# Kernel tuning notes

Measured on AMD Instinct MI355X. Metric: run time of the kernel, lower is better.

The kernel has to match this reference:

```python
import jax, jax.numpy as jnp
import numpy as np

B, C, Hs, Ws = 8, 512, 32, 32
NUM_HEADS, D_K = 8, 64
SCALE = D_K ** -0.5


def setup_inputs() -> dict:
    key = jax.random.key(0)
    ks = jax.random.split(key, 8)
    inner = NUM_HEADS * D_K  # 512
    s = 0.02
    return {
        "x": jax.random.normal(ks[0], (B, C, Hs, Ws), dtype=jnp.float32),
        "y": jax.random.normal(ks[1], (B, C, Hs, Ws), dtype=jnp.float32),
        "Wq": jax.random.normal(ks[2], (inner, C), dtype=jnp.float32) * s,
        "bq": jnp.zeros((inner,), dtype=jnp.float32),
        "Wkv": jax.random.normal(ks[3], (2 * inner, C), dtype=jnp.float32) * s,
        "bkv": jnp.zeros((2 * inner,), dtype=jnp.float32),
        "Wp": jax.random.normal(ks[4], (C, inner), dtype=jnp.float32) * s,
        "bp": jnp.zeros((C,), dtype=jnp.float32),
    }


def reference(x, y, Wq, bq, Wkv, bkv, Wp, bp):
    # Faithful to CrossAttentionBlock.forward: y is only shape-checked, unused.
    x_shape = x.shape
    b, c = x.shape[0], x.shape[1]
    # channel_transfer: [B, C, H, W] -> [B, H, W, C] -> [B, N, C]
    xt = jnp.transpose(x, (0, 2, 3, 1)).reshape(b, -1, c)
    n = xt.shape[1]
    # q: [B, N, H*dk] -> [B, H, N, dk]
    q = (xt @ Wq.T + bq).reshape(b, n, NUM_HEADS, D_K).transpose(0, 2, 1, 3)
    # kv: [B, N, 2*H*dk] -> [2, B, H, N, dk]
    kv = (xt @ Wkv.T + bkv).reshape(b, n, 2, NUM_HEADS, D_K).transpose(2, 0, 3, 1, 4)
    k, v = kv[0], kv[1]
    atten = jnp.einsum("bhik,bhjk->bhij", q, k) * SCALE
    atten = jax.nn.softmax(atten, axis=-1)
    res = jnp.einsum("bhij,bhjd->bhid", atten, v)  # [B, H, N, dk]
    res = res.transpose(0, 2, 1, 3).reshape(b, n, NUM_HEADS * D_K)
    res = res @ Wp.T + bp  # [B, N, C]
    # original does a raw reshape of [B, N, C] back into x_shape [B, C, H, W]
    return res.reshape(x_shape)
```

## Files before the change

### kernel.cpp

```cpp
#include <hip/hip_runtime.h>
#include <math.h>

#define BB 8
#define CC 512
#define NH 8
#define DK 64
#define NN 1024
#define MROWS (BB * NN)
#define INNER 512
#define SCALE 0.125f

typedef __attribute__((ext_vector_type(8))) short bf16x8;
typedef __attribute__((ext_vector_type(4))) float floatx4;

__device__ inline short f2bf(float f) {
    union { float f; unsigned u; } un;
    un.f = f;
    unsigned r = un.u + 0x7fffu + ((un.u >> 16) & 1u);
    return (short)(r >> 16);
}

__device__ inline short f2bf_rhu(float f) {
    union { float f; unsigned u; } un;
    un.f = f;
    return (short)((un.u + 0x8000u) >> 16);
}

#define GLD_LDS(gptr, lptr)                                                  \
    __builtin_amdgcn_global_load_lds(                                        \
        (const __attribute__((address_space(1))) void*)(gptr),               \
        (__attribute__((address_space(3))) void*)(lptr), 16, 0, 0)

__global__ __launch_bounds__(256) void xt_transpose_kernel(
    const float* __restrict__ x, short* __restrict__ xt) {
    __shared__ float tile[32][33];
    const int b = blockIdx.z;
    const int c0 = blockIdx.y * 32;
    const int n0 = blockIdx.x * 32;
    const float* xb = x + (size_t)b * CC * NN;
    short* xtb = xt + (size_t)b * NN * CC;
    const int tx = threadIdx.x;
    for (int i = threadIdx.y; i < 32; i += 8) {
        tile[i][tx] = xb[(size_t)(c0 + i) * NN + n0 + tx];
    }
    __syncthreads();
    for (int i = threadIdx.y; i < 32; i += 8) {
        xtb[(size_t)(n0 + i) * CC + c0 + tx] = f2bf(tile[tx][i]);
    }
}

__global__ __launch_bounds__(256) void cvt_all_kernel(
    const float* __restrict__ Wq, const float* __restrict__ Wkv,
    const float* __restrict__ Wp, const float* __restrict__ bq,
    const float* __restrict__ bkv, short* __restrict__ wqkvb,
    short* __restrict__ wpb, float* __restrict__ bqkv) {
    const int i = (blockIdx.x * 256 + threadIdx.x) * 4;
    if (i < 786432) {
        float4 v = (i < 262144) ? *(const float4*)&Wq[i]
                                : *(const float4*)&Wkv[i - 262144];
        wqkvb[i + 0] = f2bf(v.x);
        wqkvb[i + 1] = f2bf(v.y);
        wqkvb[i + 2] = f2bf(v.z);
        wqkvb[i + 3] = f2bf(v.w);
    } else if (i < 1048576) {
        const int j = i - 786432;
        float4 v = *(const float4*)&Wp[j];
        wpb[j + 0] = f2bf(v.x);
        wpb[j + 1] = f2bf(v.y);
        wpb[j + 2] = f2bf(v.z);
        wpb[j + 3] = f2bf(v.w);
    } else {
        const int j = i - 1048576;
        if (j < 1536) {
            float4 v = (j < 512) ? *(const float4*)&bq[j]
                                 : *(const float4*)&bkv[j - 512];
            *(float4*)&bqkv[j] = v;
        }
    }
}

template <int MODE>
__global__ __launch_bounds__(256) void gemm_mfma_kernel(
    const short* __restrict__ A, const short* __restrict__ W,
    const float* __restrict__ bias, float* __restrict__ outf,
    short* __restrict__ outq, short* __restrict__ outk,
    short* __restrict__ outv) {
    constexpr int K = 512;
    __shared__ short As[128 * 32];
    __shared__ short Bs[128 * 32];

    const int t = threadIdx.x;
    const int wave = t >> 6;
    const int lane = t & 63;
    const int col = lane & 15;
    const int quad = lane >> 4;
    const int wr = wave >> 1;
    const int wc = wave & 1;

    const int bm0 = blockIdx.y * 128;
    const int bn0 = blockIdx.x * 128;

    floatx4 acc[4][4];
#pragma unroll
    for (int i = 0; i < 4; i++)
#pragma unroll
        for (int j = 0; j < 4; j++) acc[i][j] = (floatx4){0.f, 0.f, 0.f, 0.f};

    const int rA = wave * 32 + (lane >> 2);
    const int kpE = (lane & 3) * 8;
    const short* Ag = A + (size_t)(bm0 + rA) * K + kpE;
    const short* Wg = W + (size_t)(bn0 + rA) * K + kpE;
    short* AsW = As + wave * 1024;
    short* BsW = Bs + wave * 1024;

    for (int k0 = 0; k0 < K; k0 += 32) {
        __syncthreads();
        GLD_LDS(Ag + k0, AsW);
        GLD_LDS(Ag + 16 * K + k0, AsW + 512);
        GLD_LDS(Wg + k0, BsW);
        GLD_LDS(Wg + 16 * K + k0, BsW + 512);
        __syncthreads();

        bf16x8 aF[4], bF[4];
#pragma unroll
        for (int rt = 0; rt < 4; rt++)
            aF[rt] = *(const bf16x8*)&As[(wr * 64 + rt * 16 + col) * 32 + quad * 8];
#pragma unroll
        for (int ct = 0; ct < 4; ct++)
            bF[ct] = *(const bf16x8*)&Bs[(wc * 64 + ct * 16 + col) * 32 + quad * 8];
#pragma unroll
        for (int rt = 0; rt < 4; rt++)
#pragma unroll
            for (int ct = 0; ct < 4; ct++)
                acc[rt][ct] = __builtin_amdgcn_mfma_f32_16x16x32_bf16(
                    aF[rt], bF[ct], acc[rt][ct], 0, 0, 0);
    }

#pragma unroll
    for (int rt = 0; rt < 4; rt++) {
#pragma unroll
        for (int ct = 0; ct < 4; ct++) {
            const int jn = bn0 + wc * 64 + ct * 16 + col;
            const float bsv = bias[jn];
#pragma unroll
            for (int r = 0; r < 4; r++) {
                const int m = bm0 + wr * 64 + rt * 16 + quad * 4 + r;
                const float val = acc[rt][ct][r] + bsv;
                if (MODE == 0) {
                    outf[(size_t)m * 512 + jn] = val;
                } else {
                    const int b = m >> 10;
                    const int n = m & 1023;
                    const int reg = jn >> 9;
                    const int h = (jn >> 6) & 7;
                    const int d = jn & 63;
                    if (reg == 0)
                        outq[(((size_t)(b * NH + h)) * NN + n) * DK + d] =
                            f2bf(val * SCALE);
                    else if (reg == 1)
                        outk[(((size_t)(b * NH + h)) * NN + n) * DK + d] = f2bf(val);
                    else
                        outv[(((size_t)(b * NH + h)) * DK + d) * NN + n] = f2bf(val);
                }
            }
        }
    }
}

__global__ __launch_bounds__(512) void attn_mfma_kernel(
    const short* __restrict__ q, const short* __restrict__ k,
    const short* __restrict__ vt, short* __restrict__ out) {
    const int bh = blockIdx.y;
    const int b = bh >> 3;
    const int h = bh & 7;
    const int n0 = blockIdx.x * 128;
    const int tid = threadIdx.x;
    const int wave = tid >> 6;
    const int lane = tid & 63;
    const int col = lane & 15;
    const int quad = lane >> 4;

    __shared__ short Ks[64 * 64];
    __shared__ short Vs[64 * 64];
    __shared__ short Ps[8][16][72];

    bf16x8 qa0, qa1;
    {
        const size_t qoff = ((size_t)bh * NN + n0 + wave * 16 + col) * DK;
        qa0 = *(const bf16x8*)&q[qoff + quad * 8];
        qa1 = *(const bf16x8*)&q[qoff + 32 + quad * 8];
    }

    floatx4 o[4];
#pragma unroll
    for (int i = 0; i < 4; i++) o[i] = (floatx4){0.f, 0.f, 0.f, 0.f};
    float l_run[4] = {0.f, 0.f, 0.f, 0.f};

    const short* kg = k + (size_t)bh * NN * DK;
    const short* vg = vt + (size_t)bh * DK * NN;

    const int srow = lane >> 3;
    const int sunit = (lane & 7) ^ srow;
    const int sbase = (wave & 3) * 16;

    const int xs = col & 7;
    const int pK0 = (quad ^ xs) * 8;
    const int pK1 = ((quad + 4) ^ xs) * 8;

    for (int j0 = 0; j0 < NN; j0 += 64) {
        __syncthreads();
        if (wave < 4) {
            GLD_LDS(kg + (size_t)(j0 + sbase + srow) * DK + sunit * 8,
                    &Ks[sbase * 64]);
            GLD_LDS(kg + (size_t)(j0 + sbase + 8 + srow) * DK + sunit * 8,
                    &Ks[(sbase + 8) * 64]);
        } else {
            GLD_LDS(vg + (size_t)(sbase + srow) * NN + j0 + sunit * 8,
                    &Vs[sbase * 64]);
            GLD_LDS(vg + (size_t)(sbase + 8 + srow) * NN + j0 + sunit * 8,
                    &Vs[(sbase + 8) * 64]);
        }
        __syncthreads();

        float p[4][4];
#pragma unroll
        for (int ct = 0; ct < 4; ct++) {
            bf16x8 kb0 = *(const bf16x8*)&Ks[(ct * 16 + col) * 64 + pK0];
            bf16x8 kb1 = *(const bf16x8*)&Ks[(ct * 16 + col) * 64 + pK1];
            floatx4 acc = (floatx4){0.f, 0.f, 0.f, 0.f};
            acc = __builtin_amdgcn_mfma_f32_16x16x32_bf16(qa0, kb0, acc, 0, 0, 0);
            acc = __builtin_amdgcn_mfma_f32_16x16x32_bf16(qa1, kb1, acc, 0, 0, 0);
#pragma unroll
            for (int r = 0; r < 4; r++) p[ct][r] = __expf(acc[r]);
        }

#pragma unroll
        for (int r = 0; r < 4; r++)
            l_run[r] += (p[0][r] + p[1][r]) + (p[2][r] + p[3][r]);

#pragma unroll
        for (int ct = 0; ct < 4; ct++)
#pragma unroll
            for (int r = 0; r < 4; r++)
                Ps[wave][quad * 4 + r][ct * 16 + col] = f2bf_rhu(p[ct][r]);

        bf16x8 pa0 = *(const bf16x8*)&Ps[wave][col][quad * 8];
        bf16x8 pa1 = *(const bf16x8*)&Ps[wave][col][32 + quad * 8];

#pragma unroll
        for (int dt = 0; dt < 4; dt++) {
            bf16x8 vb0 = *(const bf16x8*)&Vs[(dt * 16 + col) * 64 + pK0];
            bf16x8 vb1 = *(const bf16x8*)&Vs[(dt * 16 + col) * 64 + pK1];
            o[dt] = __builtin_amdgcn_mfma_f32_16x16x32_bf16(pa0, vb0, o[dt], 0, 0, 0);
            o[dt] = __builtin_amdgcn_mfma_f32_16x16x32_bf16(pa1, vb1, o[dt], 0, 0, 0);
        }
    }

#pragma unroll
    for (int r = 0; r < 4; r++) {
        float lv = l_run[r];
#pragma unroll
        for (int d = 1; d < 16; d <<= 1) lv += __shfl_xor(lv, d, 64);
        const float inv = 1.f / lv;
        const int m = n0 + wave * 16 + quad * 4 + r;
        short* orow = out + ((size_t)(b * NN + m)) * 512 + h * 64;
#pragma unroll
        for (int dt = 0; dt < 4; dt++) orow[dt * 16 + col] = f2bf(o[dt][r] * inv);
    }
}

extern "C" void kernel_launch(void* const* d_in, const int* in_sizes, int n_in,
                              void* d_out, int out_size, void* d_ws,
                              size_t ws_size, hipStream_t stream) {
    const float* x = (const float*)d_in[0];
    const float* Wq = (const float*)d_in[2];
    const float* bq = (const float*)d_in[3];
    const float* Wkv = (const float*)d_in[4];
    const float* bkv = (const float*)d_in[5];
    const float* Wp = (const float*)d_in[6];
    const float* bp = (const float*)d_in[7];
    float* out = (float*)d_out;

    short* ws = (short*)d_ws;
    short* xtb = ws;
    short* qb = xtb + (size_t)MROWS * CC;
    short* kb = qb + (size_t)MROWS * INNER;
    short* vb = kb + (size_t)MROWS * INNER;
    short* wqkvb = vb + (size_t)MROWS * INNER;
    short* wpb = wqkvb + (size_t)3 * INNER * CC;
    float* bqkv = (float*)(wpb + (size_t)CC * INNER);
    short* att = xtb;

    {
        dim3 grid(NN / 32, CC / 32, BB);
        dim3 block(32, 8);
        xt_transpose_kernel<<<grid, block, 0, stream>>>(x, xtb);
    }
    cvt_all_kernel<<<1026, 256, 0, stream>>>(Wq, Wkv, Wp, bq, bkv, wqkvb, wpb,
                                             bqkv);
    {
        dim3 grid((3 * INNER) / 128, MROWS / 128);
        gemm_mfma_kernel<1><<<grid, 256, 0, stream>>>(xtb, wqkvb, bqkv, nullptr,
                                                      qb, kb, vb);
    }
    {
        dim3 grid(NN / 128, BB * NH);
        attn_mfma_kernel<<<grid, 512, 0, stream>>>(qb, kb, vb, att);
    }
    {
        dim3 grid(CC / 128, MROWS / 128);
        gemm_mfma_kernel<0><<<grid, 256, 0, stream>>>(att, wpb, bp, out,
                                                      nullptr, nullptr, nullptr);
    }
}
```

Baseline: 171.1 us.

## Merge prep kernels, double-buffer attention K/V tiles, narrow output GEMM tile

Three separate changes. The transpose and weight-conversion kernels are merged into one launch to save a kernel launch. The attention loop double-buffers the K/V shared-memory tiles so the next tile's global-to-LDS load overlaps compute, which also removes one barrier per iteration. The output projection GEMM now uses a 64-wide N tile, doubling its grid from 256 to 512 blocks to fill more CUs, at the cost of less reuse of A per block.

```diff
diff --git a/kernel.cpp b/kernel.cpp
--- a/kernel.cpp
+++ b/kernel.cpp
@@ -31,105 +31,115 @@
         (const __attribute__((address_space(1))) void*)(gptr),               \
         (__attribute__((address_space(3))) void*)(lptr), 16, 0, 0)
 
-__global__ __launch_bounds__(256) void xt_transpose_kernel(
-    const float* __restrict__ x, short* __restrict__ xt) {
+__global__ __launch_bounds__(256) void prep_kernel(
+    const float* __restrict__ x, const float* __restrict__ Wq,
+    const float* __restrict__ Wkv, const float* __restrict__ Wp,
+    const float* __restrict__ bq, const float* __restrict__ bkv,
+    short* __restrict__ xtb, short* __restrict__ wqkvb,
+    short* __restrict__ wpb, float* __restrict__ bqkv) {
     __shared__ float tile[32][33];
-    const int b = blockIdx.z;
-    const int c0 = blockIdx.y * 32;
-    const int n0 = blockIdx.x * 32;
-    const float* xb = x + (size_t)b * CC * NN;
-    short* xtb = xt + (size_t)b * NN * CC;
-    const int tx = threadIdx.x;
-    for (int i = threadIdx.y; i < 32; i += 8) {
-        tile[i][tx] = xb[(size_t)(c0 + i) * NN + n0 + tx];
-    }
-    __syncthreads();
-    for (int i = threadIdx.y; i < 32; i += 8) {
-        xtb[(size_t)(n0 + i) * CC + c0 + tx] = f2bf(tile[tx][i]);
-    }
-}
-
-__global__ __launch_bounds__(256) void cvt_all_kernel(
-    const float* __restrict__ Wq, const float* __restrict__ Wkv,
-    const float* __restrict__ Wp, const float* __restrict__ bq,
-    const float* __restrict__ bkv, short* __restrict__ wqkvb,
-    short* __restrict__ wpb, float* __restrict__ bqkv) {
-    const int i = (blockIdx.x * 256 + threadIdx.x) * 4;
-    if (i < 786432) {
-        float4 v = (i < 262144) ? *(const float4*)&Wq[i]
-                                : *(const float4*)&Wkv[i - 262144];
-        wqkvb[i + 0] = f2bf(v.x);
-        wqkvb[i + 1] = f2bf(v.y);
-        wqkvb[i + 2] = f2bf(v.z);
-        wqkvb[i + 3] = f2bf(v.w);
-    } else if (i < 1048576) {
-        const int j = i - 786432;
-        float4 v = *(const float4*)&Wp[j];
-        wpb[j + 0] = f2bf(v.x);
-        wpb[j + 1] = f2bf(v.y);
-        wpb[j + 2] = f2bf(v.z);
-        wpb[j + 3] = f2bf(v.w);
+    const int bid = blockIdx.x;
+    if (bid < 4096) {
+        const int n0 = (bid & 31) * 32;
+        const int c0 = ((bid >> 5) & 15) * 32;
+        const int b = bid >> 9;
+        const int tx = threadIdx.x & 31;
+        const int ty = threadIdx.x >> 5;
+        const float* xb = x + (size_t)b * CC * NN;
+        short* xo = xtb + (size_t)b * NN * CC;
+        for (int i = ty; i < 32; i += 8)
+            tile[i][tx] = xb[(size_t)(c0 + i) * NN + n0 + tx];
+        __syncthreads();
+        for (int i = ty; i < 32; i += 8)
+            xo[(size_t)(n0 + i) * CC + c0 + tx] = f2bf(tile[tx][i]);
     } else {
-        const int j = i - 1048576;
-        if (j < 1536) {
-            float4 v = (j < 512) ? *(const float4*)&bq[j]
-                                 : *(const float4*)&bkv[j - 512];
-            *(float4*)&bqkv[j] = v;
-        }
-    }
-}
-
-template <int MODE>
+        const int i = (bid - 4096) * 1024 + threadIdx.x * 4;
+        if (i < 786432) {
+            float4 v = (i < 262144) ? *(const float4*)&Wq[i]
+                                    : *(const float4*)&Wkv[i - 262144];
+            wqkvb[i + 0] = f2bf(v.x);
+            wqkvb[i + 1] = f2bf(v.y);
+            wqkvb[i + 2] = f2bf(v.z);
+            wqkvb[i + 3] = f2bf(v.w);
+        } else if (i < 1048576) {
+            const int j = i - 786432;
+            float4 v = *(const float4*)&Wp[j];
+            wpb[j + 0] = f2bf(v.x);
+            wpb[j + 1] = f2bf(v.y);
+            wpb[j + 2] = f2bf(v.z);
+            wpb[j + 3] = f2bf(v.w);
+        } else {
+            const int j = i - 1048576;
+            if (j < 1536) {
+                float4 v = (j < 512) ? *(const float4*)&bq[j]
+                                     : *(const float4*)&bkv[j - 512];
+                *(float4*)&bqkv[j] = v;
+            }
+        }
+    }
+}
+
+template <int MODE, int BN>
 __global__ __launch_bounds__(256) void gemm_mfma_kernel(
     const short* __restrict__ A, const short* __restrict__ W,
     const float* __restrict__ bias, float* __restrict__ outf,
     short* __restrict__ outq, short* __restrict__ outk,
     short* __restrict__ outv) {
     constexpr int K = 512;
+    constexpr int WCOLS = BN / 64;
+    constexpr int WROWS = 4 / WCOLS;
+    constexpr int WRSPAN = 128 / WROWS;
+    constexpr int RT = WRSPAN / 16;
     __shared__ short As[128 * 32];
-    __shared__ short Bs[128 * 32];
+    __shared__ short Bs[BN * 32];
 
     const int t = threadIdx.x;
     const int wave = t >> 6;
     const int lane = t & 63;
     const int col = lane & 15;
     const int quad = lane >> 4;
-    const int wr = wave >> 1;
-    const int wc = wave & 1;
+    const int wr = wave / WCOLS;
+    const int wc = wave % WCOLS;
 
     const int bm0 = blockIdx.y * 128;
-    const int bn0 = blockIdx.x * 128;
-
-    floatx4 acc[4][4];
-#pragma unroll
-    for (int i = 0; i < 4; i++)
+    const int bn0 = blockIdx.x * BN;
+
+    floatx4 acc[RT][4];
+#pragma unroll
+    for (int i = 0; i < RT; i++)
 #pragma unroll
         for (int j = 0; j < 4; j++) acc[i][j] = (floatx4){0.f, 0.f, 0.f, 0.f};
 
+    const int kpE = (lane & 3) * 8;
     const int rA = wave * 32 + (lane >> 2);
-    const int kpE = (lane & 3) * 8;
     const short* Ag = A + (size_t)(bm0 + rA) * K + kpE;
-    const short* Wg = W + (size_t)(bn0 + rA) * K + kpE;
     short* AsW = As + wave * 1024;
-    short* BsW = Bs + wave * 1024;
+    const int rB = wave * (BN / 4) + (lane >> 2);
+    const short* Wg = W + (size_t)(bn0 + rB) * K + kpE;
+    short* BsW = Bs + wave * (BN / 4) * 32;
 
     for (int k0 = 0; k0 < K; k0 += 32) {
         __syncthreads();
         GLD_LDS(Ag + k0, AsW);
         GLD_LDS(Ag + 16 * K + k0, AsW + 512);
-        GLD_LDS(Wg + k0, BsW);
-        GLD_LDS(Wg + 16 * K + k0, BsW + 512);
+        if constexpr (BN == 128) {
+            GLD_LDS(Wg + k0, BsW);
+            GLD_LDS(Wg + 16 * K + k0, BsW + 512);
+        } else {
+            GLD_LDS(Wg + k0, BsW);
+        }
         __syncthreads();
 
-        bf16x8 aF[4], bF[4];
-#pragma unroll
-        for (int rt = 0; rt < 4; rt++)
-            aF[rt] = *(const bf16x8*)&As[(wr * 64 + rt * 16 + col) * 32 + quad * 8];
+        bf16x8 aF[RT], bF[4];
+#pragma unroll
+        for (int rt = 0; rt < RT; rt++)
+            aF[rt] =
+                *(const bf16x8*)&As[(wr * WRSPAN + rt * 16 + col) * 32 + quad * 8];
 #pragma unroll
         for (int ct = 0; ct < 4; ct++)
             bF[ct] = *(const bf16x8*)&Bs[(wc * 64 + ct * 16 + col) * 32 + quad * 8];
 #pragma unroll
-        for (int rt = 0; rt < 4; rt++)
+        for (int rt = 0; rt < RT; rt++)
 #pragma unroll
             for (int ct = 0; ct < 4; ct++)
                 acc[rt][ct] = __builtin_amdgcn_mfma_f32_16x16x32_bf16(
@@ -137,14 +147,14 @@
     }
 
 #pragma unroll
-    for (int rt = 0; rt < 4; rt++) {
+    for (int rt = 0; rt < RT; rt++) {
 #pragma unroll
         for (int ct = 0; ct < 4; ct++) {
             const int jn = bn0 + wc * 64 + ct * 16 + col;
             const float bsv = bias[jn];
 #pragma unroll
             for (int r = 0; r < 4; r++) {
-                const int m = bm0 + wr * 64 + rt * 16 + quad * 4 + r;
+                const int m = bm0 + wr * WRSPAN + rt * 16 + quad * 4 + r;
                 const float val = acc[rt][ct][r] + bsv;
                 if (MODE == 0) {
                     outf[(size_t)m * 512 + jn] = val;
@@ -180,8 +190,8 @@
     const int col = lane & 15;
     const int quad = lane >> 4;
 
-    __shared__ short Ks[64 * 64];
-    __shared__ short Vs[64 * 64];
+    __shared__ short Ks[2][64 * 64];
+    __shared__ short Vs[2][64 * 64];
     __shared__ short Ps[8][16][72];
 
     bf16x8 qa0, qa1;
@@ -207,26 +217,36 @@
     const int pK0 = (quad ^ xs) * 8;
     const int pK1 = ((quad + 4) ^ xs) * 8;
 
-    for (int j0 = 0; j0 < NN; j0 += 64) {
+#define STAGE(J0, BUF)                                                         \
+    do {                                                                       \
+        if (wave < 4) {                                                        \
+            GLD_LDS(kg + (size_t)((J0) + sbase + srow) * DK + sunit * 8,       \
+                    &Ks[BUF][sbase * 64]);                                     \
+            GLD_LDS(kg + (size_t)((J0) + sbase + 8 + srow) * DK + sunit * 8,   \
+                    &Ks[BUF][(sbase + 8) * 64]);                               \
+        } else {                                                               \
+            GLD_LDS(vg + (size_t)(sbase + srow) * NN + (J0) + sunit * 8,       \
+                    &Vs[BUF][sbase * 64]);                                     \
+            GLD_LDS(vg + (size_t)(sbase + 8 + srow) * NN + (J0) + sunit * 8,   \
+                    &Vs[BUF][(sbase + 8) * 64]);                               \
+        }                                                                      \
+    } while (0)
+
+    STAGE(0, 0);
+
+    for (int c = 0; c < 16; c++) {
+        const int buf = c & 1;
         __syncthreads();
-        if (wave < 4) {
-            GLD_LDS(kg + (size_t)(j0 + sbase + srow) * DK + sunit * 8,
-                    &Ks[sbase * 64]);
-            GLD_LDS(kg + (size_t)(j0 + sbase + 8 + srow) * DK + sunit * 8,
-                    &Ks[(sbase + 8) * 64]);
-        } else {
-            GLD_LDS(vg + (size_t)(sbase + srow) * NN + j0 + sunit * 8,
-                    &Vs[sbase * 64]);
-            GLD_LDS(vg + (size_t)(sbase + 8 + srow) * NN + j0 + sunit * 8,
-                    &Vs[(sbase + 8) * 64]);
-        }
-        __syncthreads();
+        if (c < 15) STAGE((c + 1) * 64, buf ^ 1);
+
+        const short* K_ = &Ks[buf][0];
+        const short* V_ = &Vs[buf][0];
 
         float p[4][4];
 #pragma unroll
         for (int ct = 0; ct < 4; ct++) {
-            bf16x8 kb0 = *(const bf16x8*)&Ks[(ct * 16 + col) * 64 + pK0];
-            bf16x8 kb1 = *(const bf16x8*)&Ks[(ct * 16 + col) * 64 + pK1];
+            bf16x8 kb0 = *(const bf16x8*)&K_[(ct * 16 + col) * 64 + pK0];
+            bf16x8 kb1 = *(const bf16x8*)&K_[(ct * 16 + col) * 64 + pK1];
             floatx4 acc = (floatx4){0.f, 0.f, 0.f, 0.f};
             acc = __builtin_amdgcn_mfma_f32_16x16x32_bf16(qa0, kb0, acc, 0, 0, 0);
             acc = __builtin_amdgcn_mfma_f32_16x16x32_bf16(qa1, kb1, acc, 0, 0, 0);
@@ -249,12 +269,13 @@
 
 #pragma unroll
         for (int dt = 0; dt < 4; dt++) {
-            bf16x8 vb0 = *(const bf16x8*)&Vs[(dt * 16 + col) * 64 + pK0];
-            bf16x8 vb1 = *(const bf16x8*)&Vs[(dt * 16 + col) * 64 + pK1];
+            bf16x8 vb0 = *(const bf16x8*)&V_[(dt * 16 + col) * 64 + pK0];
+            bf16x8 vb1 = *(const bf16x8*)&V_[(dt * 16 + col) * 64 + pK1];
             o[dt] = __builtin_amdgcn_mfma_f32_16x16x32_bf16(pa0, vb0, o[dt], 0, 0, 0);
             o[dt] = __builtin_amdgcn_mfma_f32_16x16x32_bf16(pa1, vb1, o[dt], 0, 0, 0);
         }
     }
+#undef STAGE
 
 #pragma unroll
     for (int r = 0; r < 4; r++) {
@@ -291,25 +312,20 @@
     float* bqkv = (float*)(wpb + (size_t)CC * INNER);
     short* att = xtb;
 
-    {
-        dim3 grid(NN / 32, CC / 32, BB);
-        dim3 block(32, 8);
-        xt_transpose_kernel<<<grid, block, 0, stream>>>(x, xtb);
-    }
-    cvt_all_kernel<<<1026, 256, 0, stream>>>(Wq, Wkv, Wp, bq, bkv, wqkvb, wpb,
-                                             bqkv);
+    prep_kernel<<<4096 + 1026, 256, 0, stream>>>(x, Wq, Wkv, Wp, bq, bkv, xtb,
+                                                 wqkvb, wpb, bqkv);
     {
         dim3 grid((3 * INNER) / 128, MROWS / 128);
-        gemm_mfma_kernel<1><<<grid, 256, 0, stream>>>(xtb, wqkvb, bqkv, nullptr,
-                                                      qb, kb, vb);
+        gemm_mfma_kernel<1, 128><<<grid, 256, 0, stream>>>(
+            xtb, wqkvb, bqkv, nullptr, qb, kb, vb);
     }
     {
         dim3 grid(NN / 128, BB * NH);
         attn_mfma_kernel<<<grid, 512, 0, stream>>>(qb, kb, vb, att);
     }
     {
-        dim3 grid(CC / 128, MROWS / 128);
-        gemm_mfma_kernel<0><<<grid, 256, 0, stream>>>(att, wpb, bp, out,
-                                                      nullptr, nullptr, nullptr);
-    }
-}
+        dim3 grid(CC / 64, MROWS / 128);
+        gemm_mfma_kernel<0, 64><<<grid, 256, 0, stream>>>(
+            att, wpb, bp, out, nullptr, nullptr, nullptr);
+    }
+}
```

After: 161.6 us. 5.5% less time.
